# Kernel tuning notes

Measured on AMD Instinct MI355X. Metric: run time of the kernel, lower is better.

Reference implementation:

```python
import jax, jax.numpy as jnp
import numpy as np

FP8_MAX = 448.0  # torch.finfo(torch.float8_e4m3fn).max

def per_tensor_quantize(t):
    amax = jnp.max(jnp.abs(t))
    scale = FP8_MAX / jnp.maximum(amax, 1e-12)
    q = jnp.clip(t * scale, -FP8_MAX, FP8_MAX).astype(jnp.float8_e4m3fn)
    return q, (1.0 / scale).astype(jnp.float32)

def fp8_gemm(q, a_scale, w_q, w_scale, out_dtype):
    # emulate: linear(A.to(out)*a_scale, B.to(out)*b_scale)
    A = q.astype(out_dtype) * a_scale
    B = w_q.astype(out_dtype) * w_scale
    return A @ B.T

def setup_inputs() -> dict:
    key = jax.random.key(0)
    k1, k2, k3, k4 = jax.random.split(key, 4)
    tokens, hidden, ffn = 4096, 4096, 10752
    return {
        "x": jax.random.normal(k1, (tokens, hidden), jnp.float32),
        "expert_w1": jax.random.normal(k2, (ffn, hidden), jnp.float32) * 0.02,
        "expert_v1": jax.random.normal(k3, (ffn, hidden), jnp.float32) * 0.02,
        "expert_w2": jax.random.normal(k4, (ffn, hidden), jnp.float32) * 0.02,
    }

def reference(x, expert_w1, expert_v1, expert_w2):
    dt = x.dtype
    # weight quantization (as done in _quantize_weights per expert)
    w1_q, w1_s = per_tensor_quantize(expert_w1)
    v1_q, v1_s = per_tensor_quantize(expert_v1)
    w2_q, w2_s = per_tensor_quantize(expert_w2)
    # activation quantization + gate/up GEMMs
    qin, x_s = per_tensor_quantize(x)
    gate = fp8_gemm(qin, x_s, w1_q, w1_s, dt)          # [N, ffn]
    up = fp8_gemm(qin, x_s, v1_q, v1_s, dt)            # [N, ffn]
    inter = jax.nn.silu(gate) * up                      # fused GLU
    qmid, m_s = per_tensor_quantize(inter)
    # down proj uses expert_w2.t() -> B = [hidden, ffn]
    down = fp8_gemm(qmid, m_s, w2_q.T, w2_s, dt)        # [N, hidden]
    return down
```

## Files before the change

kernel.cpp:

```cpp
#include <hip/hip_runtime.h>
#include <cstdint>
#include <cstddef>

typedef float f32x4 __attribute__((ext_vector_type(4)));
typedef float f32x16 __attribute__((ext_vector_type(16)));
typedef int i32x4 __attribute__((ext_vector_type(4)));
typedef int i32x8 __attribute__((ext_vector_type(8)));
typedef unsigned char u8;
typedef unsigned short u16;
typedef u16 u16x8 __attribute__((ext_vector_type(8)));
typedef unsigned int u32;
typedef u32 u32x4 __attribute__((ext_vector_type(4)));

static __device__ __forceinline__ void gload_lds16(const void* g, void* l) {
  __builtin_amdgcn_global_load_lds(
      (__attribute__((address_space(1))) void*)(void*)g,
      (__attribute__((address_space(3))) void*)l,
      16, 0, 0);
}

#if defined(__has_builtin)
#if __has_builtin(__builtin_amdgcn_cvt_pk_fp8_f32)
#define HAVE_HW_FP8 1
#endif
#endif

__device__ __forceinline__ u8 f32_to_e4m3_sw(float x) {
  unsigned s = (__float_as_uint(x) >> 24) & 0x80;
  float ax = fabsf(x);
  if (!(ax > 0.0f)) return (u8)s;
  if (ax >= 448.0f) return (u8)(s | 0x7e);
  if (ax < 0.015625f) {
    int m = (int)rintf(ax * 512.0f);
    if (m >= 8) return (u8)(s | 0x08);
    return (u8)(s | m);
  }
  int e = ilogbf(ax);
  int m = (int)rintf(ldexpf(ax, 3 - e));
  if (m == 16) { ++e; m = 8; }
  return (u8)(s | ((e + 7) << 3) | (m - 8));
}

__device__ __forceinline__ unsigned cvt4_fp8(float a, float b, float c, float d) {
#ifdef HAVE_HW_FP8
  int lo = __builtin_amdgcn_cvt_pk_fp8_f32(a, b, 0, false);
  return (unsigned)__builtin_amdgcn_cvt_pk_fp8_f32(c, d, lo, true);
#else
  return (unsigned)f32_to_e4m3_sw(a) | ((unsigned)f32_to_e4m3_sw(b) << 8) |
         ((unsigned)f32_to_e4m3_sw(c) << 16) | ((unsigned)f32_to_e4m3_sw(d) << 24);
#endif
}

__device__ __forceinline__ float clamp448(float x) {
  return fminf(fmaxf(x, -448.f), 448.f);
}

__device__ __forceinline__ u16 f32_to_bf16(float x) {
  unsigned u = __float_as_uint(x);
  return (u16)((u + 0x7FFFu + ((u >> 16) & 1u)) >> 16);
}

__global__ __launch_bounds__(256) void amax4_kernel(const float* __restrict__ x,
                                                    const float* __restrict__ w1,
                                                    const float* __restrict__ v1,
                                                    const float* __restrict__ w2,
                                                    unsigned* __restrict__ out) {
  const size_t nX = (size_t)4096 * 4096 / 4;
  const size_t nW = (size_t)10752 * 4096 / 4;
  int b = (int)blockIdx.x;
  const f32x4* p;
  size_t n4;
  int slot, b0, nb;
  if (b < 232)       { p = (const f32x4*)x;  n4 = nX; slot = 0; b0 = 0;    nb = 232; }
  else if (b < 840)  { p = (const f32x4*)w1; n4 = nW; slot = 1; b0 = 232;  nb = 608; }
  else if (b < 1448) { p = (const f32x4*)v1; n4 = nW; slot = 2; b0 = 840;  nb = 608; }
  else               { p = (const f32x4*)w2; n4 = nW; slot = 3; b0 = 1448; nb = 600; }
  float m = 0.0f;
  size_t stride = (size_t)nb * 256;
  for (size_t i = (size_t)(b - b0) * 256 + threadIdx.x; i < n4; i += stride) {
    f32x4 v = p[i];
    m = fmaxf(m, fmaxf(fmaxf(fabsf(v[0]), fabsf(v[1])), fmaxf(fabsf(v[2]), fabsf(v[3]))));
  }
#pragma unroll
  for (int off = 32; off > 0; off >>= 1) m = fmaxf(m, __shfl_down(m, off));
  __shared__ float red[4];
  int lane = threadIdx.x & 63, wid = threadIdx.x >> 6;
  if (lane == 0) red[wid] = m;
  __syncthreads();
  if (threadIdx.x == 0) {
    float v = fmaxf(fmaxf(red[0], red[1]), fmaxf(red[2], red[3]));
    atomicMax(out + slot, __float_as_uint(v));
  }
}

__global__ __launch_bounds__(256) void quant2_kernel(const float* __restrict__ w1,
                                                     u8* __restrict__ w1q,
                                                     const float* __restrict__ v1,
                                                     u8* __restrict__ v1q,
                                                     const unsigned* __restrict__ scal,
                                                     size_t n8) {
  int b = (int)blockIdx.x;
  const f32x4* p;
  uint2* q;
  float amax;
  int rb;
  if (b < 1024) { p = (const f32x4*)w1; q = (uint2*)w1q; amax = __uint_as_float(scal[1]); rb = b; }
  else          { p = (const f32x4*)v1; q = (uint2*)v1q; amax = __uint_as_float(scal[2]); rb = b - 1024; }
  float scale = 448.0f / fmaxf(amax, 1e-12f);
  size_t stride = (size_t)1024 * 256;
  for (size_t i = (size_t)rb * 256 + threadIdx.x; i < n8; i += stride) {
    f32x4 a = p[2 * i], c = p[2 * i + 1];
    uint2 r;
    r.x = cvt4_fp8(clamp448(a[0] * scale), clamp448(a[1] * scale),
                   clamp448(a[2] * scale), clamp448(a[3] * scale));
    r.y = cvt4_fp8(clamp448(c[0] * scale), clamp448(c[1] * scale),
                   clamp448(c[2] * scale), clamp448(c[3] * scale));
    q[i] = r;
  }
}

__global__ __launch_bounds__(256) void pack_f32_kernel(const float* __restrict__ src,
                                                       u8* __restrict__ dst,
                                                       const unsigned* __restrict__ amax_bits,
                                                       int K) {
  float amax = __uint_as_float(*amax_bits);
  float scale = 448.0f / fmaxf(amax, 1e-12f);
  int c = (int)blockIdx.x * 256 + (int)threadIdx.x;
  int m = c & 4095;
  int kb = c >> 12;
  const f32x4* s = (const f32x4*)(src + (size_t)m * K + kb * 32);
  unsigned w[8];
#pragma unroll
  for (int j = 0; j < 8; ++j) {
    f32x4 v = s[j];
    w[j] = cvt4_fp8(clamp448(v[0] * scale), clamp448(v[1] * scale),
                    clamp448(v[2] * scale), clamp448(v[3] * scale));
  }
  u32x4* d = (u32x4*)(dst + ((size_t)kb * 4096 + m) * 32);
  d[0] = u32x4{w[0], w[1], w[2], w[3]};
  d[1] = u32x4{w[4], w[5], w[6], w[7]};
}

__global__ __launch_bounds__(256) void pack_bf16_kernel(const u16* __restrict__ src,
                                                        u8* __restrict__ dst,
                                                        const unsigned* __restrict__ amax_bits,
                                                        int K) {
  float amax = __uint_as_float(*amax_bits);
  float scale = 448.0f / fmaxf(amax, 1e-12f);
  int c = (int)blockIdx.x * 256 + (int)threadIdx.x;
  int m = c & 4095;
  int kb = c >> 12;
  const u16x8* s = (const u16x8*)(src + (size_t)m * K + kb * 32);
  unsigned w[8];
#pragma unroll
  for (int j = 0; j < 4; ++j) {
    u16x8 v = s[j];
    float f0 = __uint_as_float((unsigned)v[0] << 16) * scale;
    float f1 = __uint_as_float((unsigned)v[1] << 16) * scale;
    float f2 = __uint_as_float((unsigned)v[2] << 16) * scale;
    float f3 = __uint_as_float((unsigned)v[3] << 16) * scale;
    float f4 = __uint_as_float((unsigned)v[4] << 16) * scale;
    float f5 = __uint_as_float((unsigned)v[5] << 16) * scale;
    float f6 = __uint_as_float((unsigned)v[6] << 16) * scale;
    float f7 = __uint_as_float((unsigned)v[7] << 16) * scale;
    w[2 * j]     = cvt4_fp8(clamp448(f0), clamp448(f1), clamp448(f2), clamp448(f3));
    w[2 * j + 1] = cvt4_fp8(clamp448(f4), clamp448(f5), clamp448(f6), clamp448(f7));
  }
  u32x4* d = (u32x4*)(dst + ((size_t)kb * 4096 + m) * 32);
  d[0] = u32x4{w[0], w[1], w[2], w[3]};
  d[1] = u32x4{w[4], w[5], w[6], w[7]};
}

__global__ __launch_bounds__(256) void quantT_kernel(const float* __restrict__ src,
                                                     u8* __restrict__ dst,
                                                     const unsigned* __restrict__ amax_bits,
                                                     int R, int C) {
  __shared__ float t[64][65];
  float amax = __uint_as_float(*amax_bits);
  float scale = 448.0f / fmaxf(amax, 1e-12f);
  int nbr = R >> 6;
  int br = (int)blockIdx.x % nbr, bc = (int)blockIdx.x / nbr;
  int r0 = br * 64, c0 = bc * 64;
  int tid = threadIdx.x;
  int lc = tid & 63, lr = tid >> 6;
#pragma unroll
  for (int i = 0; i < 16; ++i)
    t[lr + i * 4][lc] = src[(size_t)(r0 + lr + i * 4) * C + c0 + lc];
  __syncthreads();
  int qd = tid & 15, xbase = tid >> 4;
#pragma unroll
  for (int i = 0; i < 4; ++i) {
    int x = xbase + 16 * i;
    float v0 = clamp448(t[4 * qd + 0][x] * scale);
    float v1 = clamp448(t[4 * qd + 1][x] * scale);
    float v2 = clamp448(t[4 * qd + 2][x] * scale);
    float v3 = clamp448(t[4 * qd + 3][x] * scale);
    *(unsigned*)(dst + (size_t)(c0 + x) * R + r0 + 4 * qd) = cvt4_fp8(v0, v1, v2, v3);
  }
}

__device__ __forceinline__ int swz_key(int r) { return (r >> 2) & 3; }

__device__ __forceinline__ int swz_off32(int r, int h) {
  return r * 64 + ((((h << 1) ^ swz_key(r)) << 4));
}

__device__ __forceinline__ i32x8 ld_frag(const u8* base, int r, int h) {
  int o = swz_off32(r, h);
  i32x8 f;
  f.lo = *(const i32x4*)(base + o);
  f.hi = *(const i32x4*)(base + (o ^ 16));
  return f;
}

__device__ __forceinline__ i32x8 ld_a_g(const u8* p) {
  i32x8 f;
  f.lo = *(const i32x4*)p;
  f.hi = *(const i32x4*)(p + 16);
  return f;
}

#define MFMA_MX(a, b, c) \
  __builtin_amdgcn_mfma_scale_f32_32x32x64_f8f6f4((a), (b), (c), 0, 0, 0, 0x7F7F7F7F, 0, 0x7F7F7F7F)

__global__ __launch_bounds__(256, 2) void gemm1_gateup(
    const u8* __restrict__ Apk, const u8* __restrict__ Wq, const u8* __restrict__ Vq,
    const unsigned* __restrict__ scal, u16* __restrict__ inter,
    unsigned* __restrict__ amax_mid, int M, int N, int K) {
  __shared__ __align__(16) u8 lW[3][4096], lV[3][4096];
  __shared__ float red[4];
  int tid = threadIdx.x;
  int lane = tid & 63, wid = tid >> 6;
  int wm = wid >> 1, wn = wid & 1;

  int bid = (int)blockIdx.x;
  int bm = bid & 15;
  int bn = bid >> 4;

  int r0 = tid >> 2;
  int kblk = ((tid & 3) ^ swz_key(r0)) << 4;
  const u8* wS = Wq + (size_t)(bn * 64 + r0) * K + kblk;
  const u8* vS = Vq + (size_t)(bn * 64 + r0) * K + kblk;

  f32x16 g0 = (f32x16)(0.f), g1 = (f32x16)(0.f), g2 = (f32x16)(0.f), g3 = (f32x16)(0.f);
  f32x16 u0 = (f32x16)(0.f), u1 = (f32x16)(0.f), u2 = (f32x16)(0.f), u3 = (f32x16)(0.f);

  int rfrag = lane & 31;
  int h = lane >> 5;
  int arow = wm * 128 + rfrag;
  int brow = wn * 32 + rfrag;

  const size_t tStride = (size_t)64 * M;
  const u8* aP = Apk + 32 * ((size_t)M * h + (size_t)(bm * 256 + arow));

  int NT = K >> 6;
  gload_lds16(wS + 0, lW[0] + tid * 16);
  gload_lds16(vS + 0, lV[0] + tid * 16);
  gload_lds16(wS + 64, lW[1] + tid * 16);
  gload_lds16(vS + 64, lV[1] + tid * 16);
  i32x8 ac0 = ld_a_g(aP);
  i32x8 ac1 = ld_a_g(aP + 1024);
  i32x8 ac2 = ld_a_g(aP + 2048);
  i32x8 ac3 = ld_a_g(aP + 3072);
  i32x8 an0 = ac0, an1 = ac1, an2 = ac2, an3 = ac3;
  asm volatile("s_waitcnt vmcnt(0)" ::: "memory");
  __builtin_amdgcn_s_barrier();

  for (int t = 0; t < NT; ++t) {
    int cur = t % 3;
    int nx = cur + 2; if (nx >= 3) nx -= 3;
    int kt2 = (t + 2) * 64;
    bool do_stage = (t + 2) < NT;
    bool do_pref = (t + 1) < NT;
    if (do_pref) {
      asm volatile("s_waitcnt vmcnt(10)" ::: "memory");
    } else {
      asm volatile("s_waitcnt vmcnt(0)" ::: "memory");
    }
    __builtin_amdgcn_s_barrier();
    i32x8 w0 = ld_frag(lW[cur], brow, h);
    i32x8 v0 = ld_frag(lV[cur], brow, h);
    if (do_pref) {
      const u8* ap = aP + (size_t)(t + 1) * tStride;
      an0 = ld_a_g(ap);
      an1 = ld_a_g(ap + 1024);
      an2 = ld_a_g(ap + 2048);
      an3 = ld_a_g(ap + 3072);
    }
    if (do_stage) {
      gload_lds16(wS + kt2, lW[nx] + tid * 16);
      gload_lds16(vS + kt2, lV[nx] + tid * 16);
    }
    __builtin_amdgcn_s_barrier();
    __builtin_amdgcn_s_setprio(1);
    g0 = MFMA_MX(ac0, w0, g0);
    g1 = MFMA_MX(ac1, w0, g1);
    g2 = MFMA_MX(ac2, w0, g2);
    g3 = MFMA_MX(ac3, w0, g3);
    u0 = MFMA_MX(ac0, v0, u0);
    u1 = MFMA_MX(ac1, v0, u1);
    u2 = MFMA_MX(ac2, v0, u2);
    u3 = MFMA_MX(ac3, v0, u3);
    __builtin_amdgcn_s_setprio(0);
    ac0 = an0; ac1 = an1; ac2 = an2; ac3 = an3;
  }

  float ax = __uint_as_float(scal[0]);
  float aw = __uint_as_float(scal[1]);
  float av = __uint_as_float(scal[2]);
  float inv_x = 1.0f / (448.0f / fmaxf(ax, 1e-12f));
  float inv_w = 1.0f / (448.0f / fmaxf(aw, 1e-12f));
  float inv_v = 1.0f / (448.0f / fmaxf(av, 1e-12f));
  float sg = inv_x * inv_w, su = inv_x * inv_v;

  int rb = bm * 256 + wm * 128 + h * 4;
  int cb = bn * 64 + wn * 32 + rfrag;
  float lmax = 0.0f;
#pragma unroll
  for (int mi = 0; mi < 4; ++mi) {
    const f32x16& gg = mi == 0 ? g0 : mi == 1 ? g1 : mi == 2 ? g2 : g3;
    const f32x16& uu = mi == 0 ? u0 : mi == 1 ? u1 : mi == 2 ? u2 : u3;
#pragma unroll
    for (int q = 0; q < 16; ++q) {
      int rr = rb + mi * 32 + (q & 3) + 8 * (q >> 2);
      float gv = gg[q] * sg;
      float uv = uu[q] * su;
      float iv = gv / (1.0f + expf(-gv)) * uv;
      inter[(size_t)rr * N + cb] = f32_to_bf16(iv);
      lmax = fmaxf(lmax, fabsf(iv));
    }
  }
#pragma unroll
  for (int off = 32; off > 0; off >>= 1) lmax = fmaxf(lmax, __shfl_down(lmax, off));
  if (lane == 0) red[wid] = lmax;
  __syncthreads();
  if (tid == 0)
    atomicMax(amax_mid, __float_as_uint(fmaxf(fmaxf(red[0], red[1]), fmaxf(red[2], red[3]))));
}

__global__ __launch_bounds__(256, 2) void gemm2_down(
    const u8* __restrict__ Apk, const u8* __restrict__ Bq,
    const unsigned* __restrict__ amax_a, const unsigned* __restrict__ amax_b,
    float* __restrict__ out, int M, int N, int K) {
  __shared__ __align__(16) u8 lB[3][8192];
  int tid = threadIdx.x;
  int lane = tid & 63, wid = tid >> 6;
  int wm = wid >> 1, wn = wid & 1;

  int bid = (int)blockIdx.x;
  int bm = bid & 15;
  int bn = bid >> 4;

  int r0 = tid >> 2;
  int kblk = ((tid & 3) ^ swz_key(r0)) << 4;
  const u8* bS = Bq + (size_t)(bn * 128 + r0) * K + kblk;
  size_t rK = (size_t)64 * K;

  f32x16 d0 = (f32x16)(0.f), d1 = (f32x16)(0.f), d2 = (f32x16)(0.f), d3 = (f32x16)(0.f);
  f32x16 e0 = (f32x16)(0.f), e1 = (f32x16)(0.f), e2 = (f32x16)(0.f), e3 = (f32x16)(0.f);

  int rfrag = lane & 31;
  int h = lane >> 5;
  int arow = wm * 128 + rfrag;
  int brow = wn * 64 + rfrag;

  const size_t tStride = (size_t)64 * M;
  const u8* aP = Apk + 32 * ((size_t)M * h + (size_t)(bm * 256 + arow));

  int NT = K >> 6;
  gload_lds16(bS + 0, lB[0] + tid * 16);
  gload_lds16(bS + 0 + rK, lB[0] + 4096 + tid * 16);
  gload_lds16(bS + 64, lB[1] + tid * 16);
  gload_lds16(bS + 64 + rK, lB[1] + 4096 + tid * 16);
  i32x8 ac0 = ld_a_g(aP);
  i32x8 ac1 = ld_a_g(aP + 1024);
  i32x8 ac2 = ld_a_g(aP + 2048);
  i32x8 ac3 = ld_a_g(aP + 3072);
  i32x8 an0 = ac0, an1 = ac1, an2 = ac2, an3 = ac3;
  asm volatile("s_waitcnt vmcnt(0)" ::: "memory");
  __builtin_amdgcn_s_barrier();

  for (int t = 0; t < NT; ++t) {
    int cur = t % 3;
    int nx = cur + 2; if (nx >= 3) nx -= 3;
    int kt2 = (t + 2) * 64;
    bool do_stage = (t + 2) < NT;
    bool do_pref = (t + 1) < NT;
    if (do_pref) {
      asm volatile("s_waitcnt vmcnt(10)" ::: "memory");
    } else {
      asm volatile("s_waitcnt vmcnt(0)" ::: "memory");
    }
    __builtin_amdgcn_s_barrier();
    i32x8 b0 = ld_frag(lB[cur], brow, h);
    i32x8 b1 = ld_frag(lB[cur], brow + 32, h);
    if (do_pref) {
      const u8* ap = aP + (size_t)(t + 1) * tStride;
      an0 = ld_a_g(ap);
      an1 = ld_a_g(ap + 1024);
      an2 = ld_a_g(ap + 2048);
      an3 = ld_a_g(ap + 3072);
    }
    if (do_stage) {
      gload_lds16(bS + kt2, lB[nx] + tid * 16);
      gload_lds16(bS + kt2 + rK, lB[nx] + 4096 + tid * 16);
    }
    __builtin_amdgcn_s_barrier();
    __builtin_amdgcn_s_setprio(1);
    d0 = MFMA_MX(ac0, b0, d0);
    d1 = MFMA_MX(ac1, b0, d1);
    d2 = MFMA_MX(ac2, b0, d2);
    d3 = MFMA_MX(ac3, b0, d3);
    e0 = MFMA_MX(ac0, b1, e0);
    e1 = MFMA_MX(ac1, b1, e1);
    e2 = MFMA_MX(ac2, b1, e2);
    e3 = MFMA_MX(ac3, b1, e3);
    __builtin_amdgcn_s_setprio(0);
    ac0 = an0; ac1 = an1; ac2 = an2; ac3 = an3;
  }

  float sa = 1.0f / (448.0f / fmaxf(__uint_as_float(*amax_a), 1e-12f));
  float sb = 1.0f / (448.0f / fmaxf(__uint_as_float(*amax_b), 1e-12f));
  float sc = sa * sb;

  int rb = bm * 256 + wm * 128 + h * 4;
  int cb = bn * 128 + wn * 64 + rfrag;
#pragma unroll
  for (int mi = 0; mi < 4; ++mi) {
    const f32x16& dd = mi == 0 ? d0 : mi == 1 ? d1 : mi == 2 ? d2 : d3;
    const f32x16& ee = mi == 0 ? e0 : mi == 1 ? e1 : mi == 2 ? e2 : e3;
#pragma unroll
    for (int q = 0; q < 16; ++q) {
      int rr = rb + mi * 32 + (q & 3) + 8 * (q >> 2);
      out[(size_t)rr * N + cb] = dd[q] * sc;
      out[(size_t)rr * N + cb + 32] = ee[q] * sc;
    }
  }
}

extern "C" void kernel_launch(void* const* d_in, const int* in_sizes, int n_in,
                              void* d_out, int out_size, void* d_ws, size_t ws_size,
                              hipStream_t stream) {
  const float* x  = (const float*)d_in[0];
  const float* w1 = (const float*)d_in[1];
  const float* v1 = (const float*)d_in[2];
  const float* w2 = (const float*)d_in[3];
  const int M = 4096, H = 4096, F = 10752;

  u8* ws = (u8*)d_ws;
  unsigned* scal = (unsigned*)ws;
  u8* xpk  = ws + 256;
  u8* w1q  = xpk  + (size_t)M * H;
  u8* v1q  = w1q  + (size_t)F * H;
  u8* w2qT = v1q  + (size_t)F * H;
  u8* midpk = w2qT + (size_t)F * H;
  u16* inter = (u16*)(midpk + (size_t)M * F);

  hipMemsetAsync(scal, 0, 256, stream);
  amax4_kernel<<<2048, 256, 0, stream>>>(x, w1, v1, w2, scal);

  pack_f32_kernel<<<(M * (H / 32)) / 256, 256, 0, stream>>>(x, xpk, scal + 0, H);
  quant2_kernel<<<2048, 256, 0, stream>>>(w1, w1q, v1, v1q, scal, (size_t)F * H / 8);
  quantT_kernel<<<(F / 64) * (H / 64), 256, 0, stream>>>(w2, w2qT, scal + 3, F, H);

  gemm1_gateup<<<(M / 256) * (F / 64), 256, 0, stream>>>(xpk, w1q, v1q, scal, inter,
                                                         scal + 4, M, F, H);
  pack_bf16_kernel<<<(M * (F / 32)) / 256, 256, 0, stream>>>(inter, midpk, scal + 4, F);
  gemm2_down<<<(M / 256) * (H / 128), 256, 0, stream>>>(midpk, w2qT, scal + 4, scal + 3,
                                                        (float*)d_out, M, H, F);
}
```

Before: 888.4 us.

## Pre-pack weights into k-blocked layout and load B fragments directly from global

Weight quantization now writes W1, V1 and transposed W2 into the same 32-byte k-blocked packed layout already used for activations. Both GEMMs then drop the LDS triple-buffered staging, the swizzle and the barriers for B, and load B fragments straight from global memory into registers with a one-step register prefetch. This removes LDS traffic and block-wide synchronisation. In exchange, each wave now reloads B from global/L2 with no sharing through LDS, and latency is hidden only by the single-tile register prefetch.

```diff
diff --git a/kernel.cpp b/kernel.cpp
--- a/kernel.cpp
+++ b/kernel.cpp
@@ -11,13 +11,6 @@
 typedef u16 u16x8 __attribute__((ext_vector_type(8)));
 typedef unsigned int u32;
 typedef u32 u32x4 __attribute__((ext_vector_type(4)));
-
-static __device__ __forceinline__ void gload_lds16(const void* g, void* l) {
-  __builtin_amdgcn_global_load_lds(
-      (__attribute__((address_space(1))) void*)(void*)g,
-      (__attribute__((address_space(3))) void*)l,
-      16, 0, 0);
-}
 
 #if defined(__has_builtin)
 #if __has_builtin(__builtin_amdgcn_cvt_pk_fp8_f32)
@@ -93,41 +86,15 @@
   }
 }
 
-__global__ __launch_bounds__(256) void quant2_kernel(const float* __restrict__ w1,
-                                                     u8* __restrict__ w1q,
-                                                     const float* __restrict__ v1,
-                                                     u8* __restrict__ v1q,
-                                                     const unsigned* __restrict__ scal,
-                                                     size_t n8) {
-  int b = (int)blockIdx.x;
-  const f32x4* p;
-  uint2* q;
-  float amax;
-  int rb;
-  if (b < 1024) { p = (const f32x4*)w1; q = (uint2*)w1q; amax = __uint_as_float(scal[1]); rb = b; }
-  else          { p = (const f32x4*)v1; q = (uint2*)v1q; amax = __uint_as_float(scal[2]); rb = b - 1024; }
-  float scale = 448.0f / fmaxf(amax, 1e-12f);
-  size_t stride = (size_t)1024 * 256;
-  for (size_t i = (size_t)rb * 256 + threadIdx.x; i < n8; i += stride) {
-    f32x4 a = p[2 * i], c = p[2 * i + 1];
-    uint2 r;
-    r.x = cvt4_fp8(clamp448(a[0] * scale), clamp448(a[1] * scale),
-                   clamp448(a[2] * scale), clamp448(a[3] * scale));
-    r.y = cvt4_fp8(clamp448(c[0] * scale), clamp448(c[1] * scale),
-                   clamp448(c[2] * scale), clamp448(c[3] * scale));
-    q[i] = r;
-  }
-}
-
-__global__ __launch_bounds__(256) void pack_f32_kernel(const float* __restrict__ src,
-                                                       u8* __restrict__ dst,
-                                                       const unsigned* __restrict__ amax_bits,
-                                                       int K) {
+__global__ __launch_bounds__(256) void pack_f32R_kernel(const float* __restrict__ src,
+                                                        u8* __restrict__ dst,
+                                                        const unsigned* __restrict__ amax_bits,
+                                                        int R, int K) {
   float amax = __uint_as_float(*amax_bits);
   float scale = 448.0f / fmaxf(amax, 1e-12f);
   int c = (int)blockIdx.x * 256 + (int)threadIdx.x;
-  int m = c & 4095;
-  int kb = c >> 12;
+  int kb = c / R;
+  int m = c - kb * R;
   const f32x4* s = (const f32x4*)(src + (size_t)m * K + kb * 32);
   unsigned w[8];
 #pragma unroll
@@ -136,7 +103,7 @@
     w[j] = cvt4_fp8(clamp448(v[0] * scale), clamp448(v[1] * scale),
                     clamp448(v[2] * scale), clamp448(v[3] * scale));
   }
-  u32x4* d = (u32x4*)(dst + ((size_t)kb * 4096 + m) * 32);
+  u32x4* d = (u32x4*)(dst + ((size_t)kb * R + m) * 32);
   d[0] = u32x4{w[0], w[1], w[2], w[3]};
   d[1] = u32x4{w[4], w[5], w[6], w[7]};
 }
@@ -171,10 +138,10 @@
   d[1] = u32x4{w[4], w[5], w[6], w[7]};
 }
 
-__global__ __launch_bounds__(256) void quantT_kernel(const float* __restrict__ src,
-                                                     u8* __restrict__ dst,
-                                                     const unsigned* __restrict__ amax_bits,
-                                                     int R, int C) {
+__global__ __launch_bounds__(256) void packT_kernel(const float* __restrict__ src,
+                                                    u8* __restrict__ dst,
+                                                    const unsigned* __restrict__ amax_bits,
+                                                    int R, int C) {
   __shared__ float t[64][65];
   float amax = __uint_as_float(*amax_bits);
   float scale = 448.0f / fmaxf(amax, 1e-12f);
@@ -191,29 +158,18 @@
 #pragma unroll
   for (int i = 0; i < 4; ++i) {
     int x = xbase + 16 * i;
+    int n = c0 + x;
+    int k0 = r0 + 4 * qd;
     float v0 = clamp448(t[4 * qd + 0][x] * scale);
     float v1 = clamp448(t[4 * qd + 1][x] * scale);
     float v2 = clamp448(t[4 * qd + 2][x] * scale);
     float v3 = clamp448(t[4 * qd + 3][x] * scale);
-    *(unsigned*)(dst + (size_t)(c0 + x) * R + r0 + 4 * qd) = cvt4_fp8(v0, v1, v2, v3);
-  }
-}
-
-__device__ __forceinline__ int swz_key(int r) { return (r >> 2) & 3; }
-
-__device__ __forceinline__ int swz_off32(int r, int h) {
-  return r * 64 + ((((h << 1) ^ swz_key(r)) << 4));
-}
-
-__device__ __forceinline__ i32x8 ld_frag(const u8* base, int r, int h) {
-  int o = swz_off32(r, h);
-  i32x8 f;
-  f.lo = *(const i32x4*)(base + o);
-  f.hi = *(const i32x4*)(base + (o ^ 16));
-  return f;
-}
-
-__device__ __forceinline__ i32x8 ld_a_g(const u8* p) {
+    size_t addr = ((size_t)(k0 >> 5) * C + n) * 32 + (k0 & 31);
+    *(unsigned*)(dst + addr) = cvt4_fp8(v0, v1, v2, v3);
+  }
+}
+
+__device__ __forceinline__ i32x8 ld_pk(const u8* p) {
   i32x8 f;
   f.lo = *(const i32x4*)p;
   f.hi = *(const i32x4*)(p + 16);
@@ -224,10 +180,9 @@
   __builtin_amdgcn_mfma_scale_f32_32x32x64_f8f6f4((a), (b), (c), 0, 0, 0, 0x7F7F7F7F, 0, 0x7F7F7F7F)
 
 __global__ __launch_bounds__(256, 2) void gemm1_gateup(
-    const u8* __restrict__ Apk, const u8* __restrict__ Wq, const u8* __restrict__ Vq,
+    const u8* __restrict__ Apk, const u8* __restrict__ Wpk, const u8* __restrict__ Vpk,
     const unsigned* __restrict__ scal, u16* __restrict__ inter,
     unsigned* __restrict__ amax_mid, int M, int N, int K) {
-  __shared__ __align__(16) u8 lW[3][4096], lV[3][4096];
   __shared__ float red[4];
   int tid = threadIdx.x;
   int lane = tid & 63, wid = tid >> 6;
@@ -237,72 +192,51 @@
   int bm = bid & 15;
   int bn = bid >> 4;
 
-  int r0 = tid >> 2;
-  int kblk = ((tid & 3) ^ swz_key(r0)) << 4;
-  const u8* wS = Wq + (size_t)(bn * 64 + r0) * K + kblk;
-  const u8* vS = Vq + (size_t)(bn * 64 + r0) * K + kblk;
+  int rfrag = lane & 31;
+  int h = lane >> 5;
+  int arow = bm * 256 + wm * 128 + rfrag;
+  int nrow = bn * 64 + wn * 32 + rfrag;
+
+  const size_t aStep = (size_t)64 * M;
+  const size_t bStep = (size_t)64 * N;
+  const u8* aP = Apk + 32 * ((size_t)M * h + arow);
+  const u8* wP = Wpk + 32 * ((size_t)N * h + nrow);
+  const u8* vP = Vpk + 32 * ((size_t)N * h + nrow);
 
   f32x16 g0 = (f32x16)(0.f), g1 = (f32x16)(0.f), g2 = (f32x16)(0.f), g3 = (f32x16)(0.f);
   f32x16 u0 = (f32x16)(0.f), u1 = (f32x16)(0.f), u2 = (f32x16)(0.f), u3 = (f32x16)(0.f);
 
-  int rfrag = lane & 31;
-  int h = lane >> 5;
-  int arow = wm * 128 + rfrag;
-  int brow = wn * 32 + rfrag;
-
-  const size_t tStride = (size_t)64 * M;
-  const u8* aP = Apk + 32 * ((size_t)M * h + (size_t)(bm * 256 + arow));
-
   int NT = K >> 6;
-  gload_lds16(wS + 0, lW[0] + tid * 16);
-  gload_lds16(vS + 0, lV[0] + tid * 16);
-  gload_lds16(wS + 64, lW[1] + tid * 16);
-  gload_lds16(vS + 64, lV[1] + tid * 16);
-  i32x8 ac0 = ld_a_g(aP);
-  i32x8 ac1 = ld_a_g(aP + 1024);
-  i32x8 ac2 = ld_a_g(aP + 2048);
-  i32x8 ac3 = ld_a_g(aP + 3072);
-  i32x8 an0 = ac0, an1 = ac1, an2 = ac2, an3 = ac3;
-  asm volatile("s_waitcnt vmcnt(0)" ::: "memory");
-  __builtin_amdgcn_s_barrier();
+  i32x8 ac0 = ld_pk(aP);
+  i32x8 ac1 = ld_pk(aP + 1024);
+  i32x8 ac2 = ld_pk(aP + 2048);
+  i32x8 ac3 = ld_pk(aP + 3072);
+  i32x8 wc = ld_pk(wP);
+  i32x8 vc = ld_pk(vP);
 
   for (int t = 0; t < NT; ++t) {
-    int cur = t % 3;
-    int nx = cur + 2; if (nx >= 3) nx -= 3;
-    int kt2 = (t + 2) * 64;
-    bool do_stage = (t + 2) < NT;
-    bool do_pref = (t + 1) < NT;
-    if (do_pref) {
-      asm volatile("s_waitcnt vmcnt(10)" ::: "memory");
-    } else {
-      asm volatile("s_waitcnt vmcnt(0)" ::: "memory");
+    i32x8 an0 = ac0, an1 = ac1, an2 = ac2, an3 = ac3, wn_ = wc, vn_ = vc;
+    if (t + 1 < NT) {
+      const u8* ap = aP + (size_t)(t + 1) * aStep;
+      an0 = ld_pk(ap);
+      an1 = ld_pk(ap + 1024);
+      an2 = ld_pk(ap + 2048);
+      an3 = ld_pk(ap + 3072);
+      wn_ = ld_pk(wP + (size_t)(t + 1) * bStep);
+      vn_ = ld_pk(vP + (size_t)(t + 1) * bStep);
     }
-    __builtin_amdgcn_s_barrier();
-    i32x8 w0 = ld_frag(lW[cur], brow, h);
-    i32x8 v0 = ld_frag(lV[cur], brow, h);
-    if (do_pref) {
-      const u8* ap = aP + (size_t)(t + 1) * tStride;
-      an0 = ld_a_g(ap);
-      an1 = ld_a_g(ap + 1024);
-      an2 = ld_a_g(ap + 2048);
-      an3 = ld_a_g(ap + 3072);
-    }
-    if (do_stage) {
-      gload_lds16(wS + kt2, lW[nx] + tid * 16);
-      gload_lds16(vS + kt2, lV[nx] + tid * 16);
-    }
-    __builtin_amdgcn_s_barrier();
     __builtin_amdgcn_s_setprio(1);
-    g0 = MFMA_MX(ac0, w0, g0);
-    g1 = MFMA_MX(ac1, w0, g1);
-    g2 = MFMA_MX(ac2, w0, g2);
-    g3 = MFMA_MX(ac3, w0, g3);
-    u0 = MFMA_MX(ac0, v0, u0);
-    u1 = MFMA_MX(ac1, v0, u1);
-    u2 = MFMA_MX(ac2, v0, u2);
-    u3 = MFMA_MX(ac3, v0, u3);
+    g0 = MFMA_MX(ac0, wc, g0);
+    g1 = MFMA_MX(ac1, wc, g1);
+    g2 = MFMA_MX(ac2, wc, g2);
+    g3 = MFMA_MX(ac3, wc, g3);
+    u0 = MFMA_MX(ac0, vc, u0);
+    u1 = MFMA_MX(ac1, vc, u1);
+    u2 = MFMA_MX(ac2, vc, u2);
+    u3 = MFMA_MX(ac3, vc, u3);
     __builtin_amdgcn_s_setprio(0);
     ac0 = an0; ac1 = an1; ac2 = an2; ac3 = an3;
+    wc = wn_; vc = vn_;
   }
 
   float ax = __uint_as_float(scal[0]);
@@ -339,10 +273,9 @@
 }
 
 __global__ __launch_bounds__(256, 2) void gemm2_down(
-    const u8* __restrict__ Apk, const u8* __restrict__ Bq,
+    const u8* __restrict__ Apk, const u8* __restrict__ Bpk,
     const unsigned* __restrict__ amax_a, const unsigned* __restrict__ amax_b,
     float* __restrict__ out, int M, int N, int K) {
-  __shared__ __align__(16) u8 lB[3][8192];
   int tid = threadIdx.x;
   int lane = tid & 63, wid = tid >> 6;
   int wm = wid >> 1, wn = wid & 1;
@@ -351,72 +284,51 @@
   int bm = bid & 15;
   int bn = bid >> 4;
 
-  int r0 = tid >> 2;
-  int kblk = ((tid & 3) ^ swz_key(r0)) << 4;
-  const u8* bS = Bq + (size_t)(bn * 128 + r0) * K + kblk;
-  size_t rK = (size_t)64 * K;
+  int rfrag = lane & 31;
+  int h = lane >> 5;
+  int arow = bm * 256 + wm * 128 + rfrag;
+  int nrow = bn * 128 + wn * 64 + rfrag;
+
+  const size_t aStep = (size_t)64 * M;
+  const size_t bStep = (size_t)64 * N;
+  const u8* aP = Apk + 32 * ((size_t)M * h + arow);
+  const u8* bP = Bpk + 32 * ((size_t)N * h + nrow);
 
   f32x16 d0 = (f32x16)(0.f), d1 = (f32x16)(0.f), d2 = (f32x16)(0.f), d3 = (f32x16)(0.f);
   f32x16 e0 = (f32x16)(0.f), e1 = (f32x16)(0.f), e2 = (f32x16)(0.f), e3 = (f32x16)(0.f);
 
-  int rfrag = lane & 31;
-  int h = lane >> 5;
-  int arow = wm * 128 + rfrag;
-  int brow = wn * 64 + rfrag;
-
-  const size_t tStride = (size_t)64 * M;
-  const u8* aP = Apk + 32 * ((size_t)M * h + (size_t)(bm * 256 + arow));
-
   int NT = K >> 6;
-  gload_lds16(bS + 0, lB[0] + tid * 16);
-  gload_lds16(bS + 0 + rK, lB[0] + 4096 + tid * 16);
-  gload_lds16(bS + 64, lB[1] + tid * 16);
-  gload_lds16(bS + 64 + rK, lB[1] + 4096 + tid * 16);
-  i32x8 ac0 = ld_a_g(aP);
-  i32x8 ac1 = ld_a_g(aP + 1024);
-  i32x8 ac2 = ld_a_g(aP + 2048);
-  i32x8 ac3 = ld_a_g(aP + 3072);
-  i32x8 an0 = ac0, an1 = ac1, an2 = ac2, an3 = ac3;
-  asm volatile("s_waitcnt vmcnt(0)" ::: "memory");
-  __builtin_amdgcn_s_barrier();
+  i32x8 ac0 = ld_pk(aP);
+  i32x8 ac1 = ld_pk(aP + 1024);
+  i32x8 ac2 = ld_pk(aP + 2048);
+  i32x8 ac3 = ld_pk(aP + 3072);
+  i32x8 bc0 = ld_pk(bP);
+  i32x8 bc1 = ld_pk(bP + 1024);
 
   for (int t = 0; t < NT; ++t) {
-    int cur = t % 3;
-    int nx = cur + 2; if (nx >= 3) nx -= 3;
-    int kt2 = (t + 2) * 64;
-    bool do_stage = (t + 2) < NT;
-    bool do_pref = (t + 1) < NT;
-    if (do_pref) {
-      asm volatile("s_waitcnt vmcnt(10)" ::: "memory");
-    } else {
-      asm volatile("s_waitcnt vmcnt(0)" ::: "memory");
+    i32x8 an0 = ac0, an1 = ac1, an2 = ac2, an3 = ac3, bn0 = bc0, bn1 = bc1;
+    if (t + 1 < NT) {
+      const u8* ap = aP + (size_t)(t + 1) * aStep;
+      an0 = ld_pk(ap);
+      an1 = ld_pk(ap + 1024);
+      an2 = ld_pk(ap + 2048);
+      an3 = ld_pk(ap + 3072);
+      const u8* bp = bP + (size_t)(t + 1) * bStep;
+      bn0 = ld_pk(bp);
+      bn1 = ld_pk(bp + 1024);
     }
-    __builtin_amdgcn_s_barrier();
-    i32x8 b0 = ld_frag(lB[cur], brow, h);
-    i32x8 b1 = ld_frag(lB[cur], brow + 32, h);
-    if (do_pref) {
-      const u8* ap = aP + (size_t)(t + 1) * tStride;
-      an0 = ld_a_g(ap);
-      an1 = ld_a_g(ap + 1024);
-      an2 = ld_a_g(ap + 2048);
-      an3 = ld_a_g(ap + 3072);
-    }
-    if (do_stage) {
-      gload_lds16(bS + kt2, lB[nx] + tid * 16);
-      gload_lds16(bS + kt2 + rK, lB[nx] + 4096 + tid * 16);
-    }
-    __builtin_amdgcn_s_barrier();
     __builtin_amdgcn_s_setprio(1);
-    d0 = MFMA_MX(ac0, b0, d0);
-    d1 = MFMA_MX(ac1, b0, d1);
-    d2 = MFMA_MX(ac2, b0, d2);
-    d3 = MFMA_MX(ac3, b0, d3);
-    e0 = MFMA_MX(ac0, b1, e0);
-    e1 = MFMA_MX(ac1, b1, e1);
-    e2 = MFMA_MX(ac2, b1, e2);
-    e3 = MFMA_MX(ac3, b1, e3);
+    d0 = MFMA_MX(ac0, bc0, d0);
+    d1 = MFMA_MX(ac1, bc0, d1);
+    d2 = MFMA_MX(ac2, bc0, d2);
+    d3 = MFMA_MX(ac3, bc0, d3);
+    e0 = MFMA_MX(ac0, bc1, e0);
+    e1 = MFMA_MX(ac1, bc1, e1);
+    e2 = MFMA_MX(ac2, bc1, e2);
+    e3 = MFMA_MX(ac3, bc1, e3);
     __builtin_amdgcn_s_setprio(0);
     ac0 = an0; ac1 = an1; ac2 = an2; ac3 = an3;
+    bc0 = bn0; bc1 = bn1;
   }
 
   float sa = 1.0f / (448.0f / fmaxf(__uint_as_float(*amax_a), 1e-12f));
@@ -449,23 +361,24 @@
 
   u8* ws = (u8*)d_ws;
   unsigned* scal = (unsigned*)ws;
-  u8* xpk  = ws + 256;
-  u8* w1q  = xpk  + (size_t)M * H;
-  u8* v1q  = w1q  + (size_t)F * H;
-  u8* w2qT = v1q  + (size_t)F * H;
-  u8* midpk = w2qT + (size_t)F * H;
+  u8* xpk   = ws + 256;
+  u8* w1pk  = xpk  + (size_t)M * H;
+  u8* v1pk  = w1pk + (size_t)F * H;
+  u8* w2pk  = v1pk + (size_t)F * H;
+  u8* midpk = w2pk + (size_t)F * H;
   u16* inter = (u16*)(midpk + (size_t)M * F);
 
   hipMemsetAsync(scal, 0, 256, stream);
   amax4_kernel<<<2048, 256, 0, stream>>>(x, w1, v1, w2, scal);
 
-  pack_f32_kernel<<<(M * (H / 32)) / 256, 256, 0, stream>>>(x, xpk, scal + 0, H);
-  quant2_kernel<<<2048, 256, 0, stream>>>(w1, w1q, v1, v1q, scal, (size_t)F * H / 8);
-  quantT_kernel<<<(F / 64) * (H / 64), 256, 0, stream>>>(w2, w2qT, scal + 3, F, H);
-
-  gemm1_gateup<<<(M / 256) * (F / 64), 256, 0, stream>>>(xpk, w1q, v1q, scal, inter,
+  pack_f32R_kernel<<<(M * (H / 32)) / 256, 256, 0, stream>>>(x, xpk, scal + 0, M, H);
+  pack_f32R_kernel<<<(F * (H / 32)) / 256, 256, 0, stream>>>(w1, w1pk, scal + 1, F, H);
+  pack_f32R_kernel<<<(F * (H / 32)) / 256, 256, 0, stream>>>(v1, v1pk, scal + 2, F, H);
+  packT_kernel<<<(F / 64) * (H / 64), 256, 0, stream>>>(w2, w2pk, scal + 3, F, H);
+
+  gemm1_gateup<<<(M / 256) * (F / 64), 256, 0, stream>>>(xpk, w1pk, v1pk, scal, inter,
                                                          scal + 4, M, F, H);
   pack_bf16_kernel<<<(M * (F / 32)) / 256, 256, 0, stream>>>(inter, midpk, scal + 4, F);
-  gemm2_down<<<(M / 256) * (H / 128), 256, 0, stream>>>(midpk, w2qT, scal + 4, scal + 3,
+  gemm2_down<<<(M / 256) * (H / 128), 256, 0, stream>>>(midpk, w2pk, scal + 4, scal + 3,
                                                         (float*)d_out, M, H, F);
 }
```

Measured after the change: 904.1 us. No clear change (+1.8%).
